# Optimization experiments

Hardware: AMD Instinct MI355X
Metric: run time of the kernel (lower is better)

The kernel has to match this reference:

```python
import math
import jax, jax.numpy as jnp
import numpy as np

NUM_HEAD = 16


def setup_inputs() -> dict:
    key = jax.random.key(0)
    k1, k2, k3, k4 = jax.random.split(key, 4)
    B, N, E = 64, 577, 1024
    x = jax.random.normal(k1, (B, N, E), dtype=jnp.float32)
    # nn.Linear weights are [out, in]; applied as x @ W.T. Scale like torch init.
    s = 1.0 / math.sqrt(E)
    Wq = jax.random.normal(k2, (E, E), dtype=jnp.float32) * s
    Wk = jax.random.normal(k3, (E, E), dtype=jnp.float32) * s
    Wv = jax.random.normal(k4, (E, E), dtype=jnp.float32) * s
    return {"x": x, "Wq": Wq, "Wk": Wk, "Wv": Wv}


def reference(x, Wq, Wk, Wv):
    B, N, E = x.shape
    H = NUM_HEAD
    D = E // H
    # QKV projections (bias=False), split heads -> [B, H, N, D]
    def proj(W):
        return (x @ W.T).reshape(B, N, H, D).transpose(0, 2, 1, 3)
    q, k, v = proj(Wq), proj(Wk), proj(Wv)
    # scaled dot-product attention (eval mode: dropout_p = 0)
    scale = 1.0 / math.sqrt(D)
    scores = jnp.einsum("bhnd,bhmd->bhnm", q, k) * scale
    probs = jax.nn.softmax(scores, axis=-1)
    out = jnp.einsum("bhnm,bhmd->bhnd", probs, v)
    # merge heads -> [B, N, E]
    return out.transpose(0, 2, 1, 3).reshape(B, N, E)
```

## Files before the change

### kernel.cpp

```cpp
#include <hip/hip_runtime.h>
#include <hip/hip_bf16.h>


typedef __attribute__((ext_vector_type(8))) short s16x8;
typedef __attribute__((ext_vector_type(4))) float f32x4;
typedef __attribute__((ext_vector_type(16))) float f32x16;
typedef __attribute__((ext_vector_type(4))) unsigned int u32x4;
typedef __attribute__((ext_vector_type(2))) unsigned int u32x2;

#define MFMA16(a, b, c) __builtin_amdgcn_mfma_f32_16x16x32_bf16((a), (b), (c), 0, 0, 0)
#define MFMA32(a, b, c) __builtin_amdgcn_mfma_f32_32x32x16_bf16((a), (b), (c), 0, 0, 0)

__device__ __forceinline__ short f2bf(float f) {
    unsigned u = __builtin_bit_cast(unsigned, f);
    u += 0x7FFFu + ((u >> 16) & 1u);
    return (short)(u >> 16);
}

__device__ __forceinline__ unsigned cvtpk(float lo, float hi) {
    unsigned r;
    asm("v_cvt_pk_bf16_f32 %0, %1, %2" : "=v"(r) : "v"(lo), "v"(hi));
    return r;
}

__device__ __forceinline__ void gload_lds16(const void* g, void* l) {
    __builtin_amdgcn_global_load_lds(
        (const __attribute__((address_space(1))) unsigned int*)g,
        (__attribute__((address_space(3))) unsigned int*)l,
        16, 0, 0);
}

__global__ __launch_bounds__(256) void convert_bf16(
    const float* __restrict__ x,
    const float* __restrict__ Wq,
    const float* __restrict__ Wk,
    const float* __restrict__ Wv,
    short* __restrict__ xb,
    short* __restrict__ Wb)
{
    constexpr size_t NX = 37814272u / 8u;
    constexpr size_t NW = 1048576u / 8u;
    constexpr size_t NTOT = NX + 3u * NW;
    size_t stride = (size_t)gridDim.x * blockDim.x;
    for (size_t c = (size_t)blockIdx.x * blockDim.x + threadIdx.x; c < NTOT; c += stride) {
        const float* src;
        short* dst;
        size_t off;
        float scale = 1.0f;
        if (c < NX) { src = x; off = c * 8; dst = xb + off; }
        else {
            size_t cw = c - NX;
            int wsel = (int)(cw / NW);
            src = (wsel == 0) ? Wq : (wsel == 1) ? Wk : Wv;
            if (wsel == 0) scale = 0.18033688011112042f;
            off = (cw - (size_t)wsel * NW) * 8;
            dst = Wb + cw * 8;
        }
        float4 a0 = *reinterpret_cast<const float4*>(src + off);
        float4 a1 = *reinterpret_cast<const float4*>(src + off + 4);
        s16x8 v;
        v[0]=f2bf(a0.x*scale); v[1]=f2bf(a0.y*scale); v[2]=f2bf(a0.z*scale); v[3]=f2bf(a0.w*scale);
        v[4]=f2bf(a1.x*scale); v[5]=f2bf(a1.y*scale); v[6]=f2bf(a1.z*scale); v[7]=f2bf(a1.w*scale);
        *reinterpret_cast<s16x8*>(dst) = v;
    }
}

__global__ __launch_bounds__(512, 2) void qkv_gemm5(
    const short* __restrict__ xb,
    const short* __restrict__ Wb,
    short* __restrict__ Qb,
    short* __restrict__ Kb,
    short* __restrict__ Vb)
{
    constexpr int M = 36928;
    constexpr int NT = 12;
    constexpr int NWG = 145 * NT;
    __shared__ char LDS[131072];

    const int t    = threadIdx.x;
    const int lane = t & 63;
    const int w    = t >> 6;
    const int wr   = w >> 2, wc = w & 3;
    const int ml   = lane & 15, zz = lane >> 4;

    int orig = blockIdx.x;
    int xcd  = orig & 7;
    constexpr int QO = NWG / 8, RO = NWG % 8;
    int id = (xcd < RO ? xcd * (QO + 1) : RO * (QO + 1) + (xcd - RO) * QO) + (orig >> 3);
    const int tileM = (id / NT) * 256;
    const int tileN = (id % NT) * 256;

    const char* Ab = (const char*)xb;
    const char* Bb = (const char*)Wb;

    int s_row[2], s_lcol[2], s_arow[2];
    #pragma unroll
    for (int p = 0; p < 2; ++p) {
        int u = p * 512 + t;
        int row = u >> 2;
        int physu = u & 3;
        s_row[p]  = row;
        s_lcol[p] = ((physu ^ ((row >> 1) & 3)) << 4);
        int ar = tileM + row; if (ar > M - 1) ar = M - 1;
        s_arow[p] = ar;
    }

    #define REGOFF(buf_, op_, ks_) ((buf_) * 65536 + (op_) * 32768 + (ks_) * 16384)

    #define STAGE(tt_, op_, ks_, buf_)                                          \
    {   _Pragma("unroll")                                                       \
        for (int p = 0; p < 2; ++p) {                                           \
            int u = p * 512 + t;                                                \
            size_t gb;                                                          \
            if ((op_) == 0) gb = (size_t)s_arow[p] * 2048 + (tt_) * 128 + (ks_) * 64 + s_lcol[p]; \
            else            gb = (size_t)(tileN + s_row[p]) * 2048 + (tt_) * 128 + (ks_) * 64 + s_lcol[p]; \
            gload_lds16((((op_) == 0) ? Ab : Bb) + gb,                          \
                        LDS + REGOFF(buf_, op_, ks_) + u * 16);                 \
        } }

    auto rdA = [&](int buf, int ks, int mf) {
        int row = wr * 128 + mf * 16 + ml;
        int off = REGOFF(buf, 0, ks) + row * 64 + ((zz ^ ((row >> 1) & 3)) << 4);
        return *reinterpret_cast<const s16x8*>(LDS + off);
    };
    auto rdB = [&](int buf, int ks, int nf) {
        int row = wc * 64 + nf * 16 + ml;
        int off = REGOFF(buf, 1, ks) + row * 64 + ((zz ^ ((row >> 1) & 3)) << 4);
        return *reinterpret_cast<const s16x8*>(LDS + off);
    };

    #define RD_A(dst_, buf_, mb_)                                  \
    {   _Pragma("unroll")                                          \
        for (int mf2 = 0; mf2 < 4; ++mf2) {                        \
            dst_[mf2*2+0] = rdA(buf_, 0, (mb_)+mf2);               \
            dst_[mf2*2+1] = rdA(buf_, 1, (mb_)+mf2);               \
        } }
    #define RD_B(dst_, buf_, nb_)                                  \
    {   _Pragma("unroll")                                          \
        for (int nf2 = 0; nf2 < 2; ++nf2) {                        \
            dst_[nf2*2+0] = rdB(buf_, 0, (nb_)+nf2);               \
            dst_[nf2*2+1] = rdB(buf_, 1, (nb_)+nf2);               \
        } }

    #define QMFMA(AF_, BF_, MH_, NH_)                              \
    {   __builtin_amdgcn_s_setprio(1);                             \
        _Pragma("unroll")                                          \
        for (int mf2 = 0; mf2 < 4; ++mf2)                          \
            _Pragma("unroll")                                      \
            for (int nf2 = 0; nf2 < 2; ++nf2)                      \
                acc[(MH_)*4+mf2][(NH_)*2+nf2] =                    \
                    MFMA16(AF_[mf2*2+0], BF_[nf2*2+0], acc[(MH_)*4+mf2][(NH_)*2+nf2]); \
        _Pragma("unroll")                                          \
        for (int mf2 = 0; mf2 < 4; ++mf2)                          \
            _Pragma("unroll")                                      \
            for (int nf2 = 0; nf2 < 2; ++nf2)                      \
                acc[(MH_)*4+mf2][(NH_)*2+nf2] =                    \
                    MFMA16(AF_[mf2*2+1], BF_[nf2*2+1], acc[(MH_)*4+mf2][(NH_)*2+nf2]); \
        __builtin_amdgcn_s_setprio(0); }

    f32x4 acc[8][4] = {};
    s16x8 aC[8], aN[8], bC[4], bN[4];

    STAGE(0, 0, 0, 0); STAGE(0, 1, 0, 0); STAGE(0, 0, 1, 0); STAGE(0, 1, 1, 0);
    asm volatile("s_waitcnt vmcnt(0)" ::: "memory");
    __builtin_amdgcn_s_barrier();
    __builtin_amdgcn_sched_barrier(0);

    for (int tt = 0; tt < 16; ++tt) {
        const int buf = tt & 1, nbuf = buf ^ 1;
        const bool pre = (tt < 15);

        RD_A(aC, buf, 0);
        RD_B(bC, buf, 0);
        if (pre) STAGE(tt + 1, 0, 0, nbuf);
        __builtin_amdgcn_s_barrier();
        asm volatile("s_waitcnt lgkmcnt(0)" ::: "memory");
        __builtin_amdgcn_sched_barrier(0);
        QMFMA(aC, bC, 0, 0);
        __builtin_amdgcn_s_barrier();

        RD_B(bN, buf, 2);
        if (pre) STAGE(tt + 1, 1, 0, nbuf);
        __builtin_amdgcn_s_barrier();
        asm volatile("s_waitcnt lgkmcnt(0)" ::: "memory");
        __builtin_amdgcn_sched_barrier(0);
        QMFMA(aC, bN, 0, 1);
        __builtin_amdgcn_s_barrier();

        RD_A(aN, buf, 4);
        if (pre) STAGE(tt + 1, 0, 1, nbuf);
        __builtin_amdgcn_s_barrier();
        asm volatile("s_waitcnt lgkmcnt(0)" ::: "memory");
        __builtin_amdgcn_sched_barrier(0);
        QMFMA(aN, bC, 1, 0);
        __builtin_amdgcn_s_barrier();

        if (pre) STAGE(tt + 1, 1, 1, nbuf);
        __builtin_amdgcn_s_barrier();
        __builtin_amdgcn_sched_barrier(0);
        QMFMA(aN, bN, 1, 1);
        asm volatile("s_waitcnt vmcnt(0)" ::: "memory");
        __builtin_amdgcn_s_barrier();
        __builtin_amdgcn_sched_barrier(0);
    }

    const int z2 = tileN >> 10;
    short* Ob = (z2 == 0) ? Qb : (z2 == 1) ? Kb : Vb;
    const int cbase = (tileN & 1023) + wc * 64;

    #pragma unroll
    for (int mf = 0; mf < 8; ++mf) {
        #pragma unroll
        for (int j = 0; j < 4; ++j) {
            int row = tileM + wr * 128 + mf * 16 + zz * 4 + j;
            if (row < M) {
                int b = row / 577;
                int n = row - b * 577;
                #pragma unroll
                for (int nf = 0; nf < 4; ++nf) {
                    int cz = cbase + nf * 16 + ml;
                    int h = cz >> 6, dd = cz & 63;
                    Ob[(((size_t)(b * 16 + h)) * 577 + n) * 64 + dd] = f2bf(acc[mf][nf][j]);
                }
            }
        }
    }
    #undef STAGE
    #undef REGOFF
    #undef RD_A
    #undef RD_B
    #undef QMFMA
}

__global__ __launch_bounds__(256) void vtrans(
    const short* __restrict__ Vb,
    short* __restrict__ Vt)
{
    __shared__ short lds[64 * 64];
    const int t  = threadIdx.x;
    const int n0 = blockIdx.x * 64;
    const int bh = blockIdx.y;
    const size_t slab  = (size_t)bh * (577 * 64);
    const size_t vslab = (size_t)bh * (64 * 584);

    int r  = t >> 2;
    int d0 = (t & 3) * 16;
    int row = n0 + r; if (row > 576) row = 576;
    const short* src = Vb + slab + (size_t)row * 64 + d0;
    s16x8 v0 = *reinterpret_cast<const s16x8*>(src);
    s16x8 v1 = *reinterpret_cast<const s16x8*>(src + 8);
    #pragma unroll
    for (int j = 0; j < 8; ++j) {
        lds[(d0 + j) * 64 + r]     = v0[j];
        lds[(d0 + 8 + j) * 64 + r] = v1[j];
    }
    __syncthreads();
    #pragma unroll
    for (int p = 0; p < 2; ++p) {
        int u  = p * 256 + t;
        int dd = u >> 3, ns = u & 7;
        int n  = n0 + ns * 8;
        if (n < 584) {
            s16x8 vv = *reinterpret_cast<const s16x8*>(&lds[dd * 64 + ns * 8]);
            *reinterpret_cast<s16x8*>(Vt + vslab + (size_t)dd * 584 + n) = vv;
        }
    }
}

__global__ __launch_bounds__(256, 4) void attn_fwd6(
    const short* __restrict__ Qb,
    const short* __restrict__ Kb,
    const short* __restrict__ Vt,
    float* __restrict__ out)
{
    constexpr int N = 577;

    __shared__ short K_lds[2][4096];
    __shared__ short V_lds[2][4096];

    const int t     = threadIdx.x;
    const int lane  = t & 63;
    const int w     = t >> 6;
    const int col_q = lane & 31;
    const int hi    = lane >> 5;
    const int hi8   = hi * 8;
    const int c7    = col_q & 7;

    int bd  = blockIdx.x;
    int xx  = bd & 7;
    int r_  = bd >> 3;
    int qt  = r_ % 5;
    int bh  = (r_ / 5) * 8 + xx;
    const int bB = bh >> 4, hH = bh & 15;
    const size_t slab  = (size_t)bh * (N * 64);
    const size_t vslab = (size_t)bh * (64 * 584);

    const int q0 = qt * 128 + w * 32;

    s16x8 qb[4];
    {
        int qr = q0 + col_q; if (qr > N - 1) qr = N - 1;
        const short* qrow = Qb + slab + (size_t)qr * 64 + hi8;
        #pragma unroll
        for (int ks = 0; ks < 4; ++ks)
            qb[ks] = *reinterpret_cast<const s16x8*>(qrow + ks * 16);
    }

    const int sr = t >> 3;
    const int sp = t & 7;

    float m_run = -1e30f, l_run = 0.f;
    f32x16 o0 = {}, o1 = {};

    #pragma unroll
    for (int p = 0; p < 2; ++p) {
        int rr = p * 32 + sr;
        int sl = sp ^ (rr & 7);
        gload_lds16(Kb + slab + (size_t)rr * 64 + sl * 8, &K_lds[0][(rr * 8 + sp) * 8]);
        gload_lds16(Vt + vslab + (size_t)rr * 584 + sl * 8, &V_lds[0][(rr * 8 + sp) * 8]);
    }
    int cur = 0;

    for (int tile = 0; tile < 10; ++tile) {
        const int kv0 = tile * 64;
        __builtin_amdgcn_sched_barrier(0);
        __builtin_amdgcn_s_barrier();
        if (tile < 9) {
            #pragma unroll
            for (int p = 0; p < 2; ++p) {
                int rr = p * 32 + sr;
                int sl = sp ^ (rr & 7);
                gload_lds16(Kb + slab + (size_t)(kv0 + 64 + rr) * 64 + sl * 8,
                            &K_lds[cur ^ 1][(rr * 8 + sp) * 8]);
                gload_lds16(Vt + vslab + (size_t)rr * 584 + (kv0 + 64) + sl * 8,
                            &V_lds[cur ^ 1][(rr * 8 + sp) * 8]);
            }
            asm volatile("s_waitcnt vmcnt(4)" ::: "memory");
        } else {
            asm volatile("s_waitcnt vmcnt(0)" ::: "memory");
        }
        __builtin_amdgcn_sched_barrier(0);

        const short* KL = &K_lds[cur][0];
        const short* VL = &V_lds[cur][0];

        f32x16 s0 = {}, s1 = {};
        __builtin_amdgcn_s_setprio(1);
        #pragma unroll
        for (int ks = 0; ks < 4; ++ks) {
            s16x8 kf0 = *reinterpret_cast<const s16x8*>(
                KL + ((col_q * 8 + ((2*ks + hi) ^ c7)) * 8));
            s0 = MFMA32(kf0, qb[ks], s0);
        }
        #pragma unroll
        for (int ks = 0; ks < 4; ++ks) {
            s16x8 kf1 = *reinterpret_cast<const s16x8*>(
                KL + (((32 + col_q) * 8 + ((2*ks + hi) ^ c7)) * 8));
            s1 = MFMA32(kf1, qb[ks], s1);
        }
        __builtin_amdgcn_s_setprio(0);

        if (kv0 + 64 > N) {
            #pragma unroll
            for (int r = 0; r < 16; ++r) {
                int crow = (r & 3) + 8 * (r >> 2) + 4 * hi;
                if (kv0 + crow > N - 1) s0[r] = -1e30f;
                s1[r] = -1e30f;
            }
        }

        float pm = s0[0];
        #pragma unroll
        for (int r = 1; r < 15; r += 2) pm = fmaxf(fmaxf(pm, s0[r]), s0[r+1]);
        pm = fmaxf(pm, s0[15]);
        #pragma unroll
        for (int r = 0; r < 16; r += 2) pm = fmaxf(fmaxf(pm, s1[r]), s1[r+1]);
        float pmax2 = fmaxf(pm, __shfl_xor(pm, 32));

        bool need = (pmax2 - m_run) > 8.f;
        if (__ballot(need)) {
            float mn   = fmaxf(m_run, pmax2);
            float corr = exp2f(m_run - mn);
            m_run = mn;
            l_run *= corr;
            #pragma unroll
            for (int r = 0; r < 16; ++r) { o0[r] *= corr; o1[r] *= corr; }
        }
        float cmn = m_run;

        float psum = 0.f;
        #pragma unroll
        for (int r = 0; r < 16; ++r) { s0[r] = exp2f(s0[r] - cmn); psum += s0[r]; }
        #pragma unroll
        for (int r = 0; r < 16; ++r) { s1[r] = exp2f(s1[r] - cmn); psum += s1[r]; }
        l_run += psum + __shfl_xor(psum, 32);

        #define REPACK(S_, b_, dst_)                                              \
        {   u32x2 r1_ = __builtin_amdgcn_permlane32_swap(                         \
                cvtpk(S_[(b_)+0], S_[(b_)+1]), cvtpk(S_[(b_)+4], S_[(b_)+5]), false, false); \
            u32x2 r2_ = __builtin_amdgcn_permlane32_swap(                         \
                cvtpk(S_[(b_)+2], S_[(b_)+3]), cvtpk(S_[(b_)+6], S_[(b_)+7]), false, false); \
            dst_[0] = r1_[0]; dst_[2] = r1_[1]; dst_[1] = r2_[0]; dst_[3] = r2_[1]; }

        #define PVSTEP(ks_, S_, b_)                                               \
        {   u32x4 pwk_;                                                           \
            REPACK(S_, b_, pwk_);                                                 \
            s16x8 paf_ = __builtin_bit_cast(s16x8, pwk_);                         \
            s16x8 vf0_ = *reinterpret_cast<const s16x8*>(                         \
                VL + ((col_q * 8 + ((2*(ks_) + hi) ^ c7)) * 8));                  \
            o0 = MFMA32(vf0_, paf_, o0);                                          \
            s16x8 vf1_ = *reinterpret_cast<const s16x8*>(                         \
                VL + (((32 + col_q) * 8 + ((2*(ks_) + hi) ^ c7)) * 8));           \
            o1 = MFMA32(vf1_, paf_, o1);                                          \
        }

        __builtin_amdgcn_s_setprio(1);
        PVSTEP(0, s0, 0)
        PVSTEP(1, s0, 8)
        PVSTEP(2, s1, 0)
        PVSTEP(3, s1, 8)
        __builtin_amdgcn_s_setprio(0);
        #undef PVSTEP
        #undef REPACK
        cur ^= 1;
    }

    int q = q0 + col_q;
    if (q < N) {
        float inv = 1.0f / l_run;
        float* obase = out + ((size_t)bB * 577 + q) * 1024 + (size_t)hH * 64;
        #pragma unroll
        for (int gq = 0; gq < 4; ++gq) {
            float4 v0 = { o0[4*gq+0]*inv, o0[4*gq+1]*inv, o0[4*gq+2]*inv, o0[4*gq+3]*inv };
            *reinterpret_cast<float4*>(obase + 8*gq + 4*hi) = v0;
            float4 v1 = { o1[4*gq+0]*inv, o1[4*gq+1]*inv, o1[4*gq+2]*inv, o1[4*gq+3]*inv };
            *reinterpret_cast<float4*>(obase + 32 + 8*gq + 4*hi) = v1;
        }
    }
}

extern "C" void kernel_launch(void* const* d_in, const int* in_sizes, int n_in,
                              void* d_out, int out_size, void* d_ws, size_t ws_size,
                              hipStream_t stream) {
    const float* x  = (const float*)d_in[0];
    const float* Wq = (const float*)d_in[1];
    const float* Wk = (const float*)d_in[2];
    const float* Wv = (const float*)d_in[3];
    float* out = (float*)d_out;

    const size_t SZ   = (size_t)64 * 16 * 577 * 64 * 2;
    const size_t VTSZ = (size_t)1024 * 64 * 584 * 2;
    short* Qb = (short*)d_ws;
    short* Kb = (short*)((char*)d_ws + SZ);
    short* Vt = (short*)((char*)d_ws + 2 * SZ);
    short* Wb = (short*)((char*)d_ws + 2 * SZ + VTSZ);

    short* xb = (short*)d_out;
    short* Vb = (short*)((char*)d_out + SZ);

    convert_bf16<<<2048, 256, 0, stream>>>(x, Wq, Wk, Wv, xb, Wb);
    qkv_gemm5<<<dim3(145 * 12), 512, 0, stream>>>(xb, Wb, Qb, Kb, Vb);
    vtrans<<<dim3(10, 1024), 256, 0, stream>>>(Vb, Vt);
    attn_fwd6<<<5120, 256, 0, stream>>>(Qb, Kb, Vt, out);
}
```

Baseline: 487.6 us.

## Use one barrier per k-step and stagger quadrant order across waves in QKV GEMM

The QKV projection GEMM main loop is restructured so that each k-iteration waits for the previous global-to-LDS stage once, crosses a single barrier, and then issues all four prefetch stages for the next tile at the start. Before, the loop had about eight barriers per k-step. Each wave then works through the four A/B fragment quadrants in one of four rotated orders, chosen from its wave index. The aim is to cut barrier stalls and spread simultaneous LDS reads of the same fragments across waves so MFMA and LDS traffic overlap better. In exchange, waves lose lockstep coordination, all prefetches are issued as one burst, and the four unrolled orderings increase code size and may raise register pressure.

```diff
diff --git a/kernel.cpp b/kernel.cpp
--- a/kernel.cpp
+++ b/kernel.cpp
@@ -65,7 +65,7 @@
     }
 }
 
-__global__ __launch_bounds__(512, 2) void qkv_gemm5(
+__global__ __launch_bounds__(512, 2) void qkv_gemm6(
     const short* __restrict__ xb,
     const short* __restrict__ Wb,
     short* __restrict__ Qb,
@@ -82,6 +82,7 @@
     const int w    = t >> 6;
     const int wr   = w >> 2, wc = w & 3;
     const int ml   = lane & 15, zz = lane >> 4;
+    const int rot  = ((w & 4) >> 1) | (w & 1);
 
     int orig = blockIdx.x;
     int xcd  = orig & 7;
@@ -162,46 +163,54 @@
     s16x8 aC[8], aN[8], bC[4], bN[4];
 
     STAGE(0, 0, 0, 0); STAGE(0, 1, 0, 0); STAGE(0, 0, 1, 0); STAGE(0, 1, 1, 0);
-    asm volatile("s_waitcnt vmcnt(0)" ::: "memory");
-    __builtin_amdgcn_s_barrier();
-    __builtin_amdgcn_sched_barrier(0);
 
     for (int tt = 0; tt < 16; ++tt) {
         const int buf = tt & 1, nbuf = buf ^ 1;
         const bool pre = (tt < 15);
 
-        RD_A(aC, buf, 0);
-        RD_B(bC, buf, 0);
-        if (pre) STAGE(tt + 1, 0, 0, nbuf);
-        __builtin_amdgcn_s_barrier();
-        asm volatile("s_waitcnt lgkmcnt(0)" ::: "memory");
-        __builtin_amdgcn_sched_barrier(0);
-        QMFMA(aC, bC, 0, 0);
-        __builtin_amdgcn_s_barrier();
-
-        RD_B(bN, buf, 2);
-        if (pre) STAGE(tt + 1, 1, 0, nbuf);
-        __builtin_amdgcn_s_barrier();
-        asm volatile("s_waitcnt lgkmcnt(0)" ::: "memory");
-        __builtin_amdgcn_sched_barrier(0);
-        QMFMA(aC, bN, 0, 1);
-        __builtin_amdgcn_s_barrier();
-
-        RD_A(aN, buf, 4);
-        if (pre) STAGE(tt + 1, 0, 1, nbuf);
-        __builtin_amdgcn_s_barrier();
-        asm volatile("s_waitcnt lgkmcnt(0)" ::: "memory");
-        __builtin_amdgcn_sched_barrier(0);
-        QMFMA(aN, bC, 1, 0);
-        __builtin_amdgcn_s_barrier();
-
-        if (pre) STAGE(tt + 1, 1, 1, nbuf);
-        __builtin_amdgcn_s_barrier();
-        __builtin_amdgcn_sched_barrier(0);
-        QMFMA(aN, bN, 1, 1);
         asm volatile("s_waitcnt vmcnt(0)" ::: "memory");
         __builtin_amdgcn_s_barrier();
         __builtin_amdgcn_sched_barrier(0);
+        if (pre) {
+            STAGE(tt + 1, 0, 0, nbuf);
+            STAGE(tt + 1, 1, 0, nbuf);
+            STAGE(tt + 1, 0, 1, nbuf);
+            STAGE(tt + 1, 1, 1, nbuf);
+        }
+
+        if (rot == 0) {
+            RD_A(aC, buf, 0); RD_B(bC, buf, 0);
+            QMFMA(aC, bC, 0, 0);
+            RD_B(bN, buf, 2);
+            QMFMA(aC, bN, 0, 1);
+            RD_A(aN, buf, 4);
+            QMFMA(aN, bC, 1, 0);
+            QMFMA(aN, bN, 1, 1);
+        } else if (rot == 1) {
+            RD_A(aC, buf, 0); RD_B(bN, buf, 2);
+            QMFMA(aC, bN, 0, 1);
+            RD_A(aN, buf, 4);
+            QMFMA(aN, bN, 1, 1);
+            RD_B(bC, buf, 0);
+            QMFMA(aN, bC, 1, 0);
+            QMFMA(aC, bC, 0, 0);
+        } else if (rot == 2) {
+            RD_A(aN, buf, 4); RD_B(bC, buf, 0);
+            QMFMA(aN, bC, 1, 0);
+            RD_B(bN, buf, 2);
+            QMFMA(aN, bN, 1, 1);
+            RD_A(aC, buf, 0);
+            QMFMA(aC, bC, 0, 0);
+            QMFMA(aC, bN, 0, 1);
+        } else {
+            RD_A(aN, buf, 4); RD_B(bN, buf, 2);
+            QMFMA(aN, bN, 1, 1);
+            RD_B(bC, buf, 0);
+            QMFMA(aN, bC, 1, 0);
+            RD_A(aC, buf, 0);
+            QMFMA(aC, bC, 0, 0);
+            QMFMA(aC, bN, 0, 1);
+        }
     }
 
     const int z2 = tileN >> 10;
@@ -459,7 +468,7 @@
     short* Vb = (short*)((char*)d_out + SZ);
 
     convert_bf16<<<2048, 256, 0, stream>>>(x, Wq, Wk, Wv, xb, Wb);
-    qkv_gemm5<<<dim3(145 * 12), 512, 0, stream>>>(xb, Wb, Qb, Kb, Vb);
+    qkv_gemm6<<<dim3(145 * 12), 512, 0, stream>>>(xb, Wb, Qb, Kb, Vb);
     vtrans<<<dim3(10, 1024), 256, 0, stream>>>(Vb, Vt);
     attn_fwd6<<<5120, 256, 0, stream>>>(Qb, Kb, Vt, out);
 }
```

Measured after the change: 508.9 us. +4.4%, slower.
